# Optimization experiments

Hardware: AMD Instinct MI355X
Metric: run time of the kernel (lower is better)

The kernel has to match this reference:

```python
import jax, jax.numpy as jnp
import numpy as np

VOCAB = 32000
BATCH = 256
SEQ = 2048


def setup_inputs() -> dict:
    key = jax.random.key(0)
    docs = jax.random.randint(key, (BATCH, SEQ), 0, VOCAB)  # int32 token ids
    return {"docs": docs}


def reference(docs):
    # Equivalent to mean(one_hot(docs, VOCAB), axis=-2) but computed as a
    # normalized histogram via scatter-add -- never materializes the
    # [B, S, V] one-hot tensor.
    B, S = docs.shape
    rows = jnp.arange(B)[:, None]  # [B, 1] broadcast against [B, S] tokens
    hist = jnp.zeros((B, VOCAB), dtype=jnp.float32).at[rows, docs].add(1.0)
    return hist / jnp.float32(S)
```

## Files before the change

kernel.cpp:

```cpp
#include <hip/hip_runtime.h>


#define VOCAB 32000
#define BATCH 256
#define SEQ   2048
#define NCHUNK 4
#define CHUNK (VOCAB / NCHUNK)
#define BLK   512

__global__ __launch_bounds__(BLK) void bow_hist_kernel(
    const int* __restrict__ docs, float* __restrict__ out) {
    __shared__ unsigned int bins[CHUNK];

    const int wg   = blockIdx.x;
    const int b    = wg >> 2;
    const int c    = wg & (NCHUNK - 1);
    const int base = c * CHUNK;
    const int tid  = threadIdx.x;

    uint4* bins4 = reinterpret_cast<uint4*>(bins);
    for (int i = tid; i < CHUNK / 4; i += BLK) {
        bins4[i] = make_uint4(0u, 0u, 0u, 0u);
    }
    __syncthreads();

    const int4* row4 = reinterpret_cast<const int4*>(docs + (size_t)b * SEQ);
    int4 t = row4[tid];
    int r;
    r = t.x - base; if ((unsigned)r < (unsigned)CHUNK) atomicAdd(&bins[r], 1u);
    r = t.y - base; if ((unsigned)r < (unsigned)CHUNK) atomicAdd(&bins[r], 1u);
    r = t.z - base; if ((unsigned)r < (unsigned)CHUNK) atomicAdd(&bins[r], 1u);
    r = t.w - base; if ((unsigned)r < (unsigned)CHUNK) atomicAdd(&bins[r], 1u);
    __syncthreads();

    float* orow = out + (size_t)b * VOCAB + base;
    const float inv = 1.0f / (float)SEQ;
    for (int i = tid; i < CHUNK / 4; i += BLK) {
        uint4 u = bins4[i];
        float4 v;
        v.x = (float)u.x * inv;
        v.y = (float)u.y * inv;
        v.z = (float)u.z * inv;
        v.w = (float)u.w * inv;
        reinterpret_cast<float4*>(orow)[i] = v;
    }
}

extern "C" void kernel_launch(void* const* d_in, const int* in_sizes, int n_in,
                              void* d_out, int out_size, void* d_ws, size_t ws_size,
                              hipStream_t stream) {
    const int* docs = (const int*)d_in[0];
    float* out = (float*)d_out;
    bow_hist_kernel<<<dim3(BATCH * NCHUNK), dim3(BLK), 0, stream>>>(docs, out);
}
```

Baseline: 11.83 us.

## Pack histogram bins as 16-bit pairs and remap block-to-row order

Shared-memory bins are packed two 16-bit counters per 32-bit word, which halves LDS footprint and zeroing work. Counts cannot exceed SEQ=2048, so 16 bits cannot overflow. The docs load is hoisted above the bin zeroing so global latency overlaps LDS init. Blocks are remapped so that 8 consecutive rows share a chunk group, changing the order of output writes and row reuse across the chunk blocks. Occupancy may rise from the smaller LDS use, at the cost of extra unpack ALU work.

Measured after the change: 13.65 us. 15.5% more time.

```diff
diff --git a/kernel.cpp b/kernel.cpp
--- a/kernel.cpp
+++ b/kernel.cpp
@@ -10,39 +10,53 @@
 
 __global__ __launch_bounds__(BLK) void bow_hist_kernel(
     const int* __restrict__ docs, float* __restrict__ out) {
-    __shared__ unsigned int bins[CHUNK];
+    __shared__ unsigned int binsP[CHUNK / 2];
 
-    const int wg   = blockIdx.x;
-    const int b    = wg >> 2;
-    const int c    = wg & (NCHUNK - 1);
+    const int id   = blockIdx.x;
+    const int b    = ((id >> 5) << 3) + (id & 7);
+    const int c    = (id >> 3) & 3;
     const int base = c * CHUNK;
     const int tid  = threadIdx.x;
 
-    uint4* bins4 = reinterpret_cast<uint4*>(bins);
-    for (int i = tid; i < CHUNK / 4; i += BLK) {
-        bins4[i] = make_uint4(0u, 0u, 0u, 0u);
+    const int4* row4 = reinterpret_cast<const int4*>(docs + (size_t)b * SEQ);
+    int4 t = row4[tid];
+
+    uint4* binsP4 = reinterpret_cast<uint4*>(binsP);
+    for (int i = tid; i < CHUNK / 8; i += BLK) {
+        binsP4[i] = make_uint4(0u, 0u, 0u, 0u);
     }
     __syncthreads();
 
-    const int4* row4 = reinterpret_cast<const int4*>(docs + (size_t)b * SEQ);
-    int4 t = row4[tid];
     int r;
-    r = t.x - base; if ((unsigned)r < (unsigned)CHUNK) atomicAdd(&bins[r], 1u);
-    r = t.y - base; if ((unsigned)r < (unsigned)CHUNK) atomicAdd(&bins[r], 1u);
-    r = t.z - base; if ((unsigned)r < (unsigned)CHUNK) atomicAdd(&bins[r], 1u);
-    r = t.w - base; if ((unsigned)r < (unsigned)CHUNK) atomicAdd(&bins[r], 1u);
+    r = t.x - base;
+    if ((unsigned)r < (unsigned)CHUNK)
+        atomicAdd(&binsP[r >> 1], (r & 1) ? 0x10000u : 1u);
+    r = t.y - base;
+    if ((unsigned)r < (unsigned)CHUNK)
+        atomicAdd(&binsP[r >> 1], (r & 1) ? 0x10000u : 1u);
+    r = t.z - base;
+    if ((unsigned)r < (unsigned)CHUNK)
+        atomicAdd(&binsP[r >> 1], (r & 1) ? 0x10000u : 1u);
+    r = t.w - base;
+    if ((unsigned)r < (unsigned)CHUNK)
+        atomicAdd(&binsP[r >> 1], (r & 1) ? 0x10000u : 1u);
     __syncthreads();
 
     float* orow = out + (size_t)b * VOCAB + base;
     const float inv = 1.0f / (float)SEQ;
-    for (int i = tid; i < CHUNK / 4; i += BLK) {
-        uint4 u = bins4[i];
-        float4 v;
-        v.x = (float)u.x * inv;
-        v.y = (float)u.y * inv;
-        v.z = (float)u.z * inv;
-        v.w = (float)u.w * inv;
-        reinterpret_cast<float4*>(orow)[i] = v;
+    for (int i = tid; i < CHUNK / 8; i += BLK) {
+        uint4 u = binsP4[i];
+        float4 v0, v1;
+        v0.x = (float)(u.x & 0xFFFFu) * inv;
+        v0.y = (float)(u.x >> 16)     * inv;
+        v0.z = (float)(u.y & 0xFFFFu) * inv;
+        v0.w = (float)(u.y >> 16)     * inv;
+        v1.x = (float)(u.z & 0xFFFFu) * inv;
+        v1.y = (float)(u.z >> 16)     * inv;
+        v1.z = (float)(u.w & 0xFFFFu) * inv;
+        v1.w = (float)(u.w >> 16)     * inv;
+        reinterpret_cast<float4*>(orow)[i * 2 + 0] = v0;
+        reinterpret_cast<float4*>(orow)[i * 2 + 1] = v1;
     }
 }
 
```
